# Kernel tuning notes

Hardware: AMD Instinct MI355X
Metric: run time of the kernel (lower is better)

## Reference

```python
import jax, jax.numpy as jnp
import numpy as np

N, D = 8192, 512
NUM_SOURCES = 8


def setup_inputs() -> dict:
    key = jax.random.key(0)
    k1, k2, k3 = jax.random.split(key, 3)
    image_features = jax.random.normal(k1, (N, D), dtype=jnp.float32)
    text_features = jax.random.normal(k2, (N, D), dtype=jnp.float32)
    logit_scale = jnp.ones((), dtype=jnp.float32)
    source_labels = jax.random.randint(k3, (N,), 0, NUM_SOURCES, dtype=jnp.int64)
    return {
        "image_features": image_features,
        "text_features": text_features,
        "logit_scale": logit_scale,
        "source_labels": source_labels,
    }


def reference(image_features, text_features, logit_scale, source_labels):
    n = source_labels.shape[0]
    # [N, N] logits and row-wise log-softmax
    logits = logit_scale * (image_features @ text_features.T)
    log_probs = jax.nn.log_softmax(logits, axis=1)
    # same-source mask, diagonal excluded
    mask = (source_labels[:, None] == source_labels[None, :]) & (~jnp.eye(n, dtype=bool))
    count_pos = mask.sum(axis=1)  # [N]
    row_sum = jnp.where(mask, log_probs, 0.0).sum(axis=1)  # [N]
    # per-row mean over positives; rows with zero positives contribute 0
    row_mean = jnp.where(count_pos > 0, row_sum / jnp.maximum(count_pos, 1).astype(log_probs.dtype), 0.0)
    # loss = -(sum_i row_mean_i) / N
    return -row_mean.sum() / n
```

## Files before the change

### kernel.cpp

```cpp
#include <hip/hip_runtime.h>
#include <cmath>

#define NN 8192
#define DD 512
#define NSRC 8
#define PSW 8
#define COFF 100.0f

typedef __bf16 bf16x8 __attribute__((ext_vector_type(8)));
typedef float  f32x4  __attribute__((ext_vector_type(4)));

__device__ __forceinline__ unsigned short f2bf(float f) {
    unsigned u = __float_as_uint(f);
    u += 0x7fffu + ((u >> 16) & 1u);
    return (unsigned short)(u >> 16);
}

__global__ __launch_bounds__(256) void k_prep(
    const float* __restrict__ img, const float* __restrict__ txt,
    const int* __restrict__ labels,
    unsigned short* __restrict__ imgB, unsigned short* __restrict__ txtB,
    float* __restrict__ Tsum, int* __restrict__ counts)
{
    const int tid = threadIdx.x;
    if (blockIdx.x >= 128) {
        const size_t gid = (size_t)(blockIdx.x - 128) * 256 + tid;
        const size_t half = (size_t)NN * DD / 8;
        const float* src = (gid < half) ? img : txt;
        unsigned short* dst = (gid < half) ? imgB : txtB;
        const size_t off = ((gid < half) ? gid : gid - half) * 8;
        const float4 v0 = *(const float4*)(src + off);
        const float4 v1 = *(const float4*)(src + off + 4);
        union { unsigned short s[8]; uint4 v; } o;
        o.s[0] = f2bf(v0.x); o.s[1] = f2bf(v0.y); o.s[2] = f2bf(v0.z); o.s[3] = f2bf(v0.w);
        o.s[4] = f2bf(v1.x); o.s[5] = f2bf(v1.y); o.s[6] = f2bf(v1.z); o.s[7] = f2bf(v1.w);
        *(uint4*)(dst + off) = o.v;
        return;
    }
    __shared__ float Tacc[NSRC * DD];
    __shared__ int cacc[NSRC];
    const int d0 = 2 * tid;
#pragma unroll
    for (int s = 0; s < NSRC; s++) {
        Tacc[s * DD + d0] = 0.f;
        Tacc[s * DD + d0 + 1] = 0.f;
    }
    if (tid < NSRC) cacc[tid] = 0;
    __syncthreads();

    const int row0 = blockIdx.x * 64;
    if (tid < 64) atomicAdd(&cacc[labels[row0 + tid]], 1);

    for (int j = 0; j < 64; j++) {
        const int lab = labels[row0 + j];
        const float2 v = *(const float2*)(txt + (size_t)(row0 + j) * DD + d0);
        Tacc[lab * DD + d0]     += v.x;
        Tacc[lab * DD + d0 + 1] += v.y;
    }
    __syncthreads();
#pragma unroll
    for (int k = 0; k < NSRC * DD / 256; k++) {
        const int e = k * 256 + tid;
        atomicAdd(&Tsum[e], Tacc[e]);
    }
    if (tid < NSRC) atomicAdd(&counts[tid], cacc[tid]);
}

__global__ __launch_bounds__(512, 2) void k_lse_mfma256(
    const unsigned short* __restrict__ imgB, const unsigned short* __restrict__ txtB,
    const float* __restrict__ scale_p, float* __restrict__ ps)
{
    __shared__ uint4 lds[8192];
    const float scale = scale_p[0];
    const int tid  = threadIdx.x;
    const int lane = tid & 63;
    const int w    = tid >> 6;
    const int wr   = w >> 1;
    const int wc   = w & 1;
    const int lq   = lane >> 4;
    const int ln   = lane & 15;
    const int c    = blockIdx.x & 7;
    const int l    = blockIdx.x >> 3;
    const int by   = c * 4 + (l >> 3);
    const int bcg  = l & 7;
    const int row0    = by * 256;
    const int colBase = bcg * 1024;

    const int st_r  = tid >> 3;
    const int st_kc = (tid & 7) ^ (st_r & 7);
    const int xsw   = ln & 7;

    int rowA[4], colB[4][2];
#pragma unroll
    for (int ii = 0; ii < 4; ii++)
        rowA[ii] = (wr * 64 + ii * 16 + ln) * 8;
#pragma unroll
    for (int jh = 0; jh < 4; jh++)
#pragma unroll
        for (int jj = 0; jj < 2; jj++)
            colB[jh][jj] = (wc * 128 + jh * 32 + jj * 16 + ln) * 8;

#define SA(BUF, Q, T)                                                          \
    { const unsigned short* g = imgB + (size_t)(row0 + (Q) * 64 + st_r) * DD   \
          + (((T) & 7) << 6) + (st_kc << 3);                                   \
      __builtin_amdgcn_global_load_lds(                                        \
          (const __attribute__((address_space(1))) void*)g,                    \
          (__attribute__((address_space(3))) void*)                            \
              &lds[(BUF) * 4096 + (Q) * 512 + tid], 16, 0, 0); }
#define SB(BUF, Q, T)                                                          \
    { const unsigned short* g = txtB                                           \
          + (size_t)(colBase + ((((T) >> 3) & 3) << 8) + (Q) * 64 + st_r) * DD \
          + (((T) & 7) << 6) + (st_kc << 3);                                   \
      __builtin_amdgcn_global_load_lds(                                        \
          (const __attribute__((address_space(1))) void*)g,                    \
          (__attribute__((address_space(3))) void*)                            \
              &lds[(BUF) * 4096 + 2048 + (Q) * 512 + tid], 16, 0, 0); }

#define PHASE_(BUF, JH, RA, STG, VM)                                           \
    do {                                                                       \
        if (RA) {                                                              \
            _Pragma("unroll") for (int ks = 0; ks < 2; ks++)                   \
                _Pragma("unroll") for (int ii = 0; ii < 4; ii++)               \
                    af[ii][ks] = *reinterpret_cast<const bf16x8*>(             \
                        &lds[(BUF) * 4096 + rowA[ii]                           \
                             + (((ks << 2) + lq) ^ xsw)]);                     \
        }                                                                      \
        bf16x8 bf[2][2];                                                       \
        _Pragma("unroll") for (int ks = 0; ks < 2; ks++)                       \
            _Pragma("unroll") for (int jj = 0; jj < 2; jj++)                   \
                bf[jj][ks] = *reinterpret_cast<const bf16x8*>(                 \
                    &lds[(BUF) * 4096 + 2048 + colB[JH][jj]                    \
                         + (((ks << 2) + lq) ^ xsw)]);                         \
        STG;                                                                   \
        __builtin_amdgcn_s_barrier();                                          \
        asm volatile("s_waitcnt lgkmcnt(0)" ::: "memory");                     \
        __builtin_amdgcn_sched_barrier(0);                                     \
        __builtin_amdgcn_s_setprio(1);                                         \
        _Pragma("unroll") for (int ks = 0; ks < 2; ks++) {                     \
            _Pragma("unroll") for (int ii = 0; ii < 4; ii++) {                 \
                _Pragma("unroll") for (int jj = 0; jj < 2; jj++) {             \
                    acc[ii][(JH) * 2 + jj] =                                   \
                        __builtin_amdgcn_mfma_f32_16x16x32_bf16(               \
                            af[ii][ks], bf[jj][ks], acc[ii][(JH) * 2 + jj],    \
                            0, 0, 0);                                          \
                }                                                              \
            }                                                                  \
        }                                                                      \
        __builtin_amdgcn_s_setprio(0);                                         \
        if (VM) { asm volatile("s_waitcnt vmcnt(2)" ::: "memory"); }           \
        __builtin_amdgcn_s_barrier();                                          \
    } while (0)

#pragma unroll
    for (int q = 0; q < 4; q++) SA(0, q, 0);
#pragma unroll
    for (int q = 0; q < 4; q++) SB(0, q, 0);
    SA(1, 0, 1); SA(1, 2, 1);
    asm volatile("s_waitcnt vmcnt(2)" ::: "memory");
    __builtin_amdgcn_s_barrier();

    f32x4 acc[4][8];
    f32x4 s_run[4];
#pragma unroll
    for (int i = 0; i < 4; i++) {
        s_run[i] = (f32x4){0.f, 0.f, 0.f, 0.f};
#pragma unroll
        for (int j = 0; j < 8; j++) acc[i][j] = (f32x4){0.f, 0.f, 0.f, 0.f};
    }
    bf16x8 af[4][2];

#pragma unroll 1
    for (int v0 = 0; v0 < 32; v0 += 2) {
        PHASE_(0, 0, 1,
               SA(1, 1, v0 + 1); SA(1, 3, v0 + 1);
               SB(1, 0, v0 + 1); SB(1, 1, v0 + 1);
               SB(1, 2, v0 + 1); SB(1, 3, v0 + 1), 0);
        PHASE_(0, 1, 0, (void)0, 0);
        PHASE_(0, 2, 0, SA(0, 0, v0 + 2); SA(0, 2, v0 + 2), 0);
        PHASE_(0, 3, 0, (void)0, 1);
        PHASE_(1, 0, 1,
               SA(0, 1, v0 + 2); SA(0, 3, v0 + 2);
               SB(0, 0, v0 + 2); SB(0, 1, v0 + 2);
               SB(0, 2, v0 + 2); SB(0, 3, v0 + 2), 0);
        PHASE_(1, 1, 0, (void)0, 0);
        PHASE_(1, 2, 0, SA(1, 0, v0 + 3); SA(1, 2, v0 + 3), 0);
        PHASE_(1, 3, 0, (void)0, 1);
        if ((v0 & 6) == 6) {
#pragma unroll
            for (int i = 0; i < 4; i++) {
#pragma unroll
                for (int rg = 0; rg < 4; rg++) {
                    float es = s_run[i][rg];
#pragma unroll
                    for (int j = 0; j < 8; j++)
                        es += __expf(fmaf(acc[i][j][rg], scale, -COFF));
                    s_run[i][rg] = es;
                }
#pragma unroll
                for (int j = 0; j < 8; j++)
                    acc[i][j] = (f32x4){0.f, 0.f, 0.f, 0.f};
            }
        }
    }

    asm volatile("s_waitcnt vmcnt(0)" ::: "memory");
    __syncthreads();

    float* fred = (float*)lds;
#pragma unroll
    for (int i = 0; i < 4; i++) {
#pragma unroll
        for (int rg = 0; rg < 4; rg++) {
            float es = s_run[i][rg];
#pragma unroll
            for (int off = 8; off; off >>= 1) es += __shfl_xor(es, off);
            if (ln == 0)
                fred[(wr * 64 + i * 16 + lq * 4 + rg) * 2 + wc] = es;
        }
    }
    __syncthreads();
    if (tid < 256) {
        const float tot = fred[tid * 2] + fred[tid * 2 + 1];
        ps[(size_t)(row0 + tid) * PSW + bcg] = tot;
    }
#undef SA
#undef SB
#undef PHASE_
}

__global__ __launch_bounds__(256) void k_finalize(
    const float* __restrict__ img, const float* __restrict__ txt,
    const int* __restrict__ labels, const float* __restrict__ scale_p,
    const float* __restrict__ Tsum, const int* __restrict__ counts,
    const float* __restrict__ ps,
    float* __restrict__ out)
{
    const float scale = scale_p[0];
    const int tid = threadIdx.x;
    const int lane = tid & 63;
    const int wave = tid >> 6;
    const int rowBase = blockIdx.x * 16 + wave * 4;
    float local = 0.f;
#pragma unroll
    for (int it = 0; it < 4; it++) {
        const int i = rowBase + it;
        const int lab = labels[i];
        float ds = 0.f, dt = 0.f;
        const float* ip = img + (size_t)i * DD;
        const float* tp = txt + (size_t)i * DD;
        const float* sp = Tsum + lab * DD;
#pragma unroll
        for (int k = lane; k < DD; k += 64) {
            const float a = ip[k];
            ds = fmaf(a, tp[k], ds);
            dt = fmaf(a, sp[k], dt);
        }
        float es = (lane < PSW) ? ps[(size_t)i * PSW + lane] : 0.f;
#pragma unroll
        for (int off = 32; off; off >>= 1) {
            ds += __shfl_xor(ds, off);
            dt += __shfl_xor(dt, off);
            es += __shfl_xor(es, off);
        }
        if (lane == 0) {
            const float lse = COFF + __logf(es);
            const int cnt = counts[lab] - 1;
            if (cnt > 0) {
                const float row_sum = scale * (dt - ds) - (float)cnt * lse;
                local += row_sum / (float)cnt;
            }
        }
    }
    __shared__ float red[4];
    if (lane == 0) red[wave] = local;
    __syncthreads();
    if (tid == 0) {
        const float t = red[0] + red[1] + red[2] + red[3];
        atomicAdd(out, -t / (float)NN);
    }
}

extern "C" void kernel_launch(void* const* d_in, const int* in_sizes, int n_in,
                              void* d_out, int out_size, void* d_ws, size_t ws_size,
                              hipStream_t stream)
{
    const float* img     = (const float*)d_in[0];
    const float* txt     = (const float*)d_in[1];
    const float* scale_p = (const float*)d_in[2];
    const int*   labels  = (const int*)d_in[3];
    float* out = (float*)d_out;

    char* ws = (char*)d_ws;
    float* ps    = (float*)(ws);
    float* Tsum  = (float*)(ws + (1 << 18));
    int*   counts = (int*)(ws + (1 << 18) + NSRC * DD * 4);
    unsigned short* imgB = (unsigned short*)(ws + 2 * 1024 * 1024);
    unsigned short* txtB = (unsigned short*)(ws + 10 * 1024 * 1024);

    hipMemsetAsync(ws + (1 << 18), 0, NSRC * DD * 4 + 64, stream);
    hipMemsetAsync(d_out, 0, 4, stream);

    k_prep<<<128 + (2 * NN * DD / 8) / 256, 256, 0, stream>>>(
        img, txt, labels, imgB, txtB, Tsum, counts);
    k_lse_mfma256<<<256, 512, 0, stream>>>(imgB, txtB, scale_p, ps);
    k_finalize<<<NN / 16, 256, 0, stream>>>(img, txt, labels, scale_p,
                                            Tsum, counts, ps, out);
}
```

Before: 165.5 us.

## Fuse diagonal dot into bf16 conversion, merge MFMA phases, read bf16 in finalize

The bf16 conversion pass now works one row per wave and also computes the diagonal image·text dot product in fp32, storing it so the finalize kernel no longer rereads both fp32 matrices. Finalize reads the bf16 image row instead of fp32 to compute the dot with the per-source sum, which halves that traffic but uses rounded image values. The GEMM main loop merges four B-column phases into two larger phases per buffer, with precomputed byte offsets and base pointers, so there are fewer barriers but more registers held for B fragments.

```diff
diff --git a/kernel.cpp b/kernel.cpp
--- a/kernel.cpp
+++ b/kernel.cpp
@@ -20,21 +20,31 @@
     const float* __restrict__ img, const float* __restrict__ txt,
     const int* __restrict__ labels,
     unsigned short* __restrict__ imgB, unsigned short* __restrict__ txtB,
-    float* __restrict__ Tsum, int* __restrict__ counts)
+    float* __restrict__ Tsum, int* __restrict__ counts,
+    float* __restrict__ dsv)
 {
     const int tid = threadIdx.x;
     if (blockIdx.x >= 128) {
-        const size_t gid = (size_t)(blockIdx.x - 128) * 256 + tid;
-        const size_t half = (size_t)NN * DD / 8;
-        const float* src = (gid < half) ? img : txt;
-        unsigned short* dst = (gid < half) ? imgB : txtB;
-        const size_t off = ((gid < half) ? gid : gid - half) * 8;
-        const float4 v0 = *(const float4*)(src + off);
-        const float4 v1 = *(const float4*)(src + off + 4);
-        union { unsigned short s[8]; uint4 v; } o;
-        o.s[0] = f2bf(v0.x); o.s[1] = f2bf(v0.y); o.s[2] = f2bf(v0.z); o.s[3] = f2bf(v0.w);
-        o.s[4] = f2bf(v1.x); o.s[5] = f2bf(v1.y); o.s[6] = f2bf(v1.z); o.s[7] = f2bf(v1.w);
-        *(uint4*)(dst + off) = o.v;
+        const int wv   = tid >> 6;
+        const int lane = tid & 63;
+        const int row  = (blockIdx.x - 128) * 4 + wv;
+        const size_t base = (size_t)row * DD + lane * 8;
+        const float4 i0 = *(const float4*)(img + base);
+        const float4 i1 = *(const float4*)(img + base + 4);
+        const float4 t0 = *(const float4*)(txt + base);
+        const float4 t1 = *(const float4*)(txt + base + 4);
+        union { unsigned short s[8]; uint4 v; } oi, ot;
+        oi.s[0] = f2bf(i0.x); oi.s[1] = f2bf(i0.y); oi.s[2] = f2bf(i0.z); oi.s[3] = f2bf(i0.w);
+        oi.s[4] = f2bf(i1.x); oi.s[5] = f2bf(i1.y); oi.s[6] = f2bf(i1.z); oi.s[7] = f2bf(i1.w);
+        ot.s[0] = f2bf(t0.x); ot.s[1] = f2bf(t0.y); ot.s[2] = f2bf(t0.z); ot.s[3] = f2bf(t0.w);
+        ot.s[4] = f2bf(t1.x); ot.s[5] = f2bf(t1.y); ot.s[6] = f2bf(t1.z); ot.s[7] = f2bf(t1.w);
+        *(uint4*)(imgB + base) = oi.v;
+        *(uint4*)(txtB + base) = ot.v;
+        float ds = i0.x * t0.x + i0.y * t0.y + i0.z * t0.z + i0.w * t0.w
+                 + i1.x * t1.x + i1.y * t1.y + i1.z * t1.z + i1.w * t1.w;
+#pragma unroll
+        for (int off = 32; off; off >>= 1) ds += __shfl_xor(ds, off);
+        if (lane == 0) dsv[row] = ds;
         return;
     }
     __shared__ float Tacc[NSRC * DD];
@@ -90,47 +100,47 @@
     const int st_kc = (tid & 7) ^ (st_r & 7);
     const int xsw   = ln & 7;
 
-    int rowA[4], colB[4][2];
-#pragma unroll
-    for (int ii = 0; ii < 4; ii++)
-        rowA[ii] = (wr * 64 + ii * 16 + ln) * 8;
-#pragma unroll
-    for (int jh = 0; jh < 4; jh++)
-#pragma unroll
-        for (int jj = 0; jj < 2; jj++)
-            colB[jh][jj] = (wc * 128 + jh * 32 + jj * 16 + ln) * 8;
+    int aA[2][2], aB[2][2];
+#pragma unroll
+    for (int b = 0; b < 2; b++)
+#pragma unroll
+        for (int ks = 0; ks < 2; ks++) {
+            const int perm = ((ks << 2) + lq) ^ xsw;
+            aA[b][ks] = b * 65536 + ((wr * 64 + ln) * 8 + perm) * 16;
+            aB[b][ks] = b * 65536 + 32768 + ((wc * 128 + ln) * 8 + perm) * 16;
+        }
+    const unsigned short* gA0 = imgB + (size_t)(row0 + st_r) * DD + (st_kc << 3);
+    const unsigned short* gB0 = txtB + (size_t)(colBase + st_r) * DD + (st_kc << 3);
 
 #define SA(BUF, Q, T)                                                          \
-    { const unsigned short* g = imgB + (size_t)(row0 + (Q) * 64 + st_r) * DD   \
-          + (((T) & 7) << 6) + (st_kc << 3);                                   \
+    { const unsigned short* g = gA0 + ((Q) << 15) + (((T) & 7) << 6);          \
       __builtin_amdgcn_global_load_lds(                                        \
           (const __attribute__((address_space(1))) void*)g,                    \
           (__attribute__((address_space(3))) void*)                            \
               &lds[(BUF) * 4096 + (Q) * 512 + tid], 16, 0, 0); }
 #define SB(BUF, Q, T)                                                          \
-    { const unsigned short* g = txtB                                           \
-          + (size_t)(colBase + ((((T) >> 3) & 3) << 8) + (Q) * 64 + st_r) * DD \
-          + (((T) & 7) << 6) + (st_kc << 3);                                   \
+    { const unsigned short* g = gB0 + ((size_t)(((T) >> 3) & 3) << 17)         \
+          + ((Q) << 15) + (((T) & 7) << 6);                                    \
       __builtin_amdgcn_global_load_lds(                                        \
           (const __attribute__((address_space(1))) void*)g,                    \
           (__attribute__((address_space(3))) void*)                            \
               &lds[(BUF) * 4096 + 2048 + (Q) * 512 + tid], 16, 0, 0); }
 
-#define PHASE_(BUF, JH, RA, STG, VM)                                           \
+#define PH_(BUF, HALF, STG, VM)                                                \
     do {                                                                       \
-        if (RA) {                                                              \
+        if (!(HALF)) {                                                         \
             _Pragma("unroll") for (int ks = 0; ks < 2; ks++)                   \
                 _Pragma("unroll") for (int ii = 0; ii < 4; ii++)               \
                     af[ii][ks] = *reinterpret_cast<const bf16x8*>(             \
-                        &lds[(BUF) * 4096 + rowA[ii]                           \
-                             + (((ks << 2) + lq) ^ xsw)]);                     \
+                        (const char*)lds + aA[BUF][ks] + ii * 2048);           \
         }                                                                      \
-        bf16x8 bf[2][2];                                                       \
+        bf16x8 bf[2][2][2];                                                    \
         _Pragma("unroll") for (int ks = 0; ks < 2; ks++)                       \
-            _Pragma("unroll") for (int jj = 0; jj < 2; jj++)                   \
-                bf[jj][ks] = *reinterpret_cast<const bf16x8*>(                 \
-                    &lds[(BUF) * 4096 + 2048 + colB[JH][jj]                    \
-                         + (((ks << 2) + lq) ^ xsw)]);                         \
+            _Pragma("unroll") for (int j2 = 0; j2 < 2; j2++)                   \
+                _Pragma("unroll") for (int jj = 0; jj < 2; jj++)               \
+                    bf[j2][jj][ks] = *reinterpret_cast<const bf16x8*>(         \
+                        (const char*)lds + aB[BUF][ks]                         \
+                        + ((HALF) * 2 + j2) * 4096 + jj * 2048);               \
         STG;                                                                   \
         __builtin_amdgcn_s_barrier();                                          \
         asm volatile("s_waitcnt lgkmcnt(0)" ::: "memory");                     \
@@ -138,11 +148,13 @@
         __builtin_amdgcn_s_setprio(1);                                         \
         _Pragma("unroll") for (int ks = 0; ks < 2; ks++) {                     \
             _Pragma("unroll") for (int ii = 0; ii < 4; ii++) {                 \
-                _Pragma("unroll") for (int jj = 0; jj < 2; jj++) {             \
-                    acc[ii][(JH) * 2 + jj] =                                   \
-                        __builtin_amdgcn_mfma_f32_16x16x32_bf16(               \
-                            af[ii][ks], bf[jj][ks], acc[ii][(JH) * 2 + jj],    \
-                            0, 0, 0);                                          \
+                _Pragma("unroll") for (int j2 = 0; j2 < 2; j2++) {             \
+                    _Pragma("unroll") for (int jj = 0; jj < 2; jj++) {         \
+                        acc[ii][((HALF) * 2 + j2) * 2 + jj] =                  \
+                            __builtin_amdgcn_mfma_f32_16x16x32_bf16(           \
+                                af[ii][ks], bf[j2][jj][ks],                    \
+                                acc[ii][((HALF) * 2 + j2) * 2 + jj], 0, 0, 0); \
+                    }                                                          \
                 }                                                              \
             }                                                                  \
         }                                                                      \
@@ -171,20 +183,16 @@
 
 #pragma unroll 1
     for (int v0 = 0; v0 < 32; v0 += 2) {
-        PHASE_(0, 0, 1,
-               SA(1, 1, v0 + 1); SA(1, 3, v0 + 1);
-               SB(1, 0, v0 + 1); SB(1, 1, v0 + 1);
-               SB(1, 2, v0 + 1); SB(1, 3, v0 + 1), 0);
-        PHASE_(0, 1, 0, (void)0, 0);
-        PHASE_(0, 2, 0, SA(0, 0, v0 + 2); SA(0, 2, v0 + 2), 0);
-        PHASE_(0, 3, 0, (void)0, 1);
-        PHASE_(1, 0, 1,
-               SA(0, 1, v0 + 2); SA(0, 3, v0 + 2);
-               SB(0, 0, v0 + 2); SB(0, 1, v0 + 2);
-               SB(0, 2, v0 + 2); SB(0, 3, v0 + 2), 0);
-        PHASE_(1, 1, 0, (void)0, 0);
-        PHASE_(1, 2, 0, SA(1, 0, v0 + 3); SA(1, 2, v0 + 3), 0);
-        PHASE_(1, 3, 0, (void)0, 1);
+        PH_(0, 0,
+            SA(1, 1, v0 + 1); SA(1, 3, v0 + 1);
+            SB(1, 0, v0 + 1); SB(1, 1, v0 + 1);
+            SB(1, 2, v0 + 1); SB(1, 3, v0 + 1), 0);
+        PH_(0, 1, SA(0, 0, v0 + 2); SA(0, 2, v0 + 2), 1);
+        PH_(1, 0,
+            SA(0, 1, v0 + 2); SA(0, 3, v0 + 2);
+            SB(0, 0, v0 + 2); SB(0, 1, v0 + 2);
+            SB(0, 2, v0 + 2); SB(0, 3, v0 + 2), 0);
+        PH_(1, 1, SA(1, 0, v0 + 3); SA(1, 2, v0 + 3), 1);
         if ((v0 & 6) == 6) {
 #pragma unroll
             for (int i = 0; i < 4; i++) {
@@ -225,14 +233,14 @@
     }
 #undef SA
 #undef SB
-#undef PHASE_
+#undef PH_
 }
 
 __global__ __launch_bounds__(256) void k_finalize(
-    const float* __restrict__ img, const float* __restrict__ txt,
+    const unsigned short* __restrict__ imgB,
     const int* __restrict__ labels, const float* __restrict__ scale_p,
     const float* __restrict__ Tsum, const int* __restrict__ counts,
-    const float* __restrict__ ps,
+    const float* __restrict__ ps, const float* __restrict__ dsv,
     float* __restrict__ out)
 {
     const float scale = scale_p[0];
@@ -245,20 +253,23 @@
     for (int it = 0; it < 4; it++) {
         const int i = rowBase + it;
         const int lab = labels[i];
-        float ds = 0.f, dt = 0.f;
-        const float* ip = img + (size_t)i * DD;
-        const float* tp = txt + (size_t)i * DD;
-        const float* sp = Tsum + lab * DD;
-#pragma unroll
-        for (int k = lane; k < DD; k += 64) {
-            const float a = ip[k];
-            ds = fmaf(a, tp[k], ds);
-            dt = fmaf(a, sp[k], dt);
-        }
+        const float* sp = Tsum + lab * DD + lane * 8;
+        union { uint4 v; unsigned short s[8]; } iv;
+        iv.v = *(const uint4*)(imgB + (size_t)i * DD + lane * 8);
+        const float4 s0 = *(const float4*)(sp);
+        const float4 s1 = *(const float4*)(sp + 4);
+        float dt = 0.f;
+        dt = fmaf(__uint_as_float((unsigned)iv.s[0] << 16), s0.x, dt);
+        dt = fmaf(__uint_as_float((unsigned)iv.s[1] << 16), s0.y, dt);
+        dt = fmaf(__uint_as_float((unsigned)iv.s[2] << 16), s0.z, dt);
+        dt = fmaf(__uint_as_float((unsigned)iv.s[3] << 16), s0.w, dt);
+        dt = fmaf(__uint_as_float((unsigned)iv.s[4] << 16), s1.x, dt);
+        dt = fmaf(__uint_as_float((unsigned)iv.s[5] << 16), s1.y, dt);
+        dt = fmaf(__uint_as_float((unsigned)iv.s[6] << 16), s1.z, dt);
+        dt = fmaf(__uint_as_float((unsigned)iv.s[7] << 16), s1.w, dt);
         float es = (lane < PSW) ? ps[(size_t)i * PSW + lane] : 0.f;
 #pragma unroll
         for (int off = 32; off; off >>= 1) {
-            ds += __shfl_xor(ds, off);
             dt += __shfl_xor(dt, off);
             es += __shfl_xor(es, off);
         }
@@ -266,7 +277,7 @@
             const float lse = COFF + __logf(es);
             const int cnt = counts[lab] - 1;
             if (cnt > 0) {
-                const float row_sum = scale * (dt - ds) - (float)cnt * lse;
+                const float row_sum = scale * (dt - dsv[i]) - (float)cnt * lse;
                 local += row_sum / (float)cnt;
             }
         }
@@ -294,15 +305,16 @@
     float* ps    = (float*)(ws);
     float* Tsum  = (float*)(ws + (1 << 18));
     int*   counts = (int*)(ws + (1 << 18) + NSRC * DD * 4);
+    float* dsv   = (float*)(ws + 0x48000);
     unsigned short* imgB = (unsigned short*)(ws + 2 * 1024 * 1024);
     unsigned short* txtB = (unsigned short*)(ws + 10 * 1024 * 1024);
 
     hipMemsetAsync(ws + (1 << 18), 0, NSRC * DD * 4 + 64, stream);
     hipMemsetAsync(d_out, 0, 4, stream);
 
-    k_prep<<<128 + (2 * NN * DD / 8) / 256, 256, 0, stream>>>(
-        img, txt, labels, imgB, txtB, Tsum, counts);
+    k_prep<<<128 + NN / 4, 256, 0, stream>>>(
+        img, txt, labels, imgB, txtB, Tsum, counts, dsv);
     k_lse_mfma256<<<256, 512, 0, stream>>>(imgB, txtB, scale_p, ps);
-    k_finalize<<<NN / 16, 256, 0, stream>>>(img, txt, labels, scale_p,
-                                            Tsum, counts, ps, out);
-}
+    k_finalize<<<NN / 16, 256, 0, stream>>>(imgB, labels, scale_p,
+                                            Tsum, counts, ps, dsv, out);
+}
```

Measured after the change: 158.6 us. 1.04x faster.
